# Performance work log

Hardware: AMD Instinct MI355X
Metric: run time of the kernel (lower is better)

The kernel has to match this reference:

```python
import jax, jax.numpy as jnp
import numpy as np

N, M, D = 8192, 8192, 256

def setup_inputs() -> dict:
    key = jax.random.key(0)
    kx, ky = jax.random.split(key)
    x = jax.random.normal(kx, (N, D), dtype=jnp.float32)
    y = jax.random.normal(ky, (M, D), dtype=jnp.float32)
    gamma = jnp.float32(1.0)  # learnable scalar parameter
    return {"x": x, "y": y, "gamma": gamma}

def reference(x, y, gamma):
    # Flatten trailing dims (matches x.view(x.size(0), -1))
    x = x.reshape(x.shape[0], -1)
    y = y.reshape(y.shape[0], -1)
    x_sq = jnp.sum(x * x, axis=-1)  # [N]
    y_sq = jnp.sum(y * y, axis=-1)  # [M]
    xy = x @ y.T                    # [N, M]
    sqdist = jnp.maximum(x_sq[:, None] + y_sq[None, :] - 2.0 * xy, 0.0)
    return jnp.exp(-gamma * sqdist)
```

## Files before the change

### kernel.cpp

```cpp
#include <hip/hip_runtime.h>
#include <stdint.h>


typedef __attribute__((ext_vector_type(4))) float f32x4;
typedef __attribute__((ext_vector_type(8))) int   i32x8;

#define NN 8192
#define MM 8192
#define DD 256
#define BK 128

__global__ __launch_bounds__(256) void prep_kernel(
    const float* __restrict__ x, const float* __restrict__ y,
    unsigned char* __restrict__ xb, unsigned char* __restrict__ yb,
    float* __restrict__ xsq, float* __restrict__ ysq) {
  const int lane = threadIdx.x & 63;
  const int row  = blockIdx.x * 4 + (threadIdx.x >> 6);

  const float* src = x;
  unsigned char* dst = xb;
  float* sq = xsq;
  int r = row;
  if (row >= NN) { src = y; dst = yb; sq = ysq; r = row - NN; }

  const float4 v = reinterpret_cast<const float4*>(src + (size_t)r * DD)[lane];
  float s = v.x * v.x + v.y * v.y + v.z * v.z + v.w * v.w;

  int w = 0;
  w = __builtin_amdgcn_cvt_pk_fp8_f32(v.x, v.y, w, false);
  w = __builtin_amdgcn_cvt_pk_fp8_f32(v.z, v.w, w, true);
  reinterpret_cast<int*>(dst + (size_t)r * DD)[lane] = w;

  #pragma unroll
  for (int o = 32; o > 0; o >>= 1) s += __shfl_down(s, o);
  if (lane == 0) sq[r] = s;
}

__global__ __launch_bounds__(256, 2) void rbf_gemm_kernel(
    const unsigned char* __restrict__ xb, const unsigned char* __restrict__ yb,
    const float* __restrict__ xsq, const float* __restrict__ ysq,
    const float* __restrict__ gamma, float* __restrict__ out) {
  __shared__ unsigned char As[128 * BK];
  __shared__ unsigned char Bs[128 * BK];

  const int tid   = threadIdx.x;
  const int lane  = tid & 63;
  const int wave  = tid >> 6;
  const int waveM = wave >> 1;
  const int waveN = wave & 1;
  const int row0  = blockIdx.y * 128;
  const int col0  = blockIdx.x * 128;

  f32x4 acc[4][4] = {};

  const int srow = lane >> 3;
  const int spos = lane & 7;
  const int sseg = ((spos & 1) | (((spos >> 1) ^ (srow & 3)) << 1)) * 16;

  const int fm = lane & 15;
  const int g  = lane >> 4;
  const int foff = fm * 128 + ((g ^ (fm & 3)) * 32);

  #pragma unroll
  for (int kt = 0; kt < 2; ++kt) {
    const int kk = kt * BK;
    __syncthreads();
    #pragma unroll
    for (int q = 0; q < 2; ++q) {
      const int c = wave * 2 + q;
      #pragma unroll
      for (int p = 0; p < 2; ++p) {
        const unsigned char* ga =
            yb + (size_t)(col0 + c * 16 + p * 8 + srow) * DD + kk + sseg;
        __builtin_amdgcn_global_load_lds(
            (const __attribute__((address_space(1))) void*)ga,
            (__attribute__((address_space(3))) void*)(As + c * 2048 + p * 1024),
            16, 0, 0);
        const unsigned char* gb =
            xb + (size_t)(row0 + c * 16 + p * 8 + srow) * DD + kk + sseg;
        __builtin_amdgcn_global_load_lds(
            (const __attribute__((address_space(1))) void*)gb,
            (__attribute__((address_space(3))) void*)(Bs + c * 2048 + p * 1024),
            16, 0, 0);
      }
    }
    __syncthreads();

    i32x8 a[4], b[4];
    #pragma unroll
    for (int i = 0; i < 4; ++i)
      a[i] = *reinterpret_cast<const i32x8*>(As + (waveM * 4 + i) * 2048 + foff);
    #pragma unroll
    for (int j = 0; j < 4; ++j)
      b[j] = *reinterpret_cast<const i32x8*>(Bs + (waveN * 4 + j) * 2048 + foff);

    #pragma unroll
    for (int i = 0; i < 4; ++i)
      #pragma unroll
      for (int j = 0; j < 4; ++j)
        acc[i][j] = __builtin_amdgcn_mfma_scale_f32_16x16x128_f8f6f4(
            a[i], b[j], acc[i][j], 0, 0,
            0, 0x7F7F7F7F, 0, 0x7F7F7F7F);
  }

  const float gm = gamma[0];
  const int rowb = row0 + waveN * 64 + (lane & 15);
  const int colq = col0 + waveM * 64 + (lane >> 4) * 4;

  float xsv[4];
  #pragma unroll
  for (int j = 0; j < 4; ++j) xsv[j] = xsq[rowb + j * 16];
  float4 ysv[4];
  #pragma unroll
  for (int i = 0; i < 4; ++i)
    ysv[i] = *reinterpret_cast<const float4*>(ysq + colq + i * 16);

  #pragma unroll
  for (int j = 0; j < 4; ++j) {
    const size_t obase = (size_t)(rowb + j * 16) * MM;
    #pragma unroll
    for (int i = 0; i < 4; ++i) {
      const float s0 = xsv[j] + ysv[i].x - 2.0f * acc[i][j][0];
      const float s1 = xsv[j] + ysv[i].y - 2.0f * acc[i][j][1];
      const float s2 = xsv[j] + ysv[i].z - 2.0f * acc[i][j][2];
      const float s3 = xsv[j] + ysv[i].w - 2.0f * acc[i][j][3];
      float4 v;
      const float mn = fminf(fminf(s0, s1), fminf(s2, s3));
      if (gm * mn >= 105.0f) {
        v.x = 0.0f; v.y = 0.0f; v.z = 0.0f; v.w = 0.0f;
      } else {
        v.x = __expf(-gm * fmaxf(s0, 0.0f));
        v.y = __expf(-gm * fmaxf(s1, 0.0f));
        v.z = __expf(-gm * fmaxf(s2, 0.0f));
        v.w = __expf(-gm * fmaxf(s3, 0.0f));
      }
      *reinterpret_cast<float4*>(out + obase + colq + i * 16) = v;
    }
  }
}

extern "C" void kernel_launch(void* const* d_in, const int* in_sizes, int n_in,
                              void* d_out, int out_size, void* d_ws, size_t ws_size,
                              hipStream_t stream) {
  const float* x     = (const float*)d_in[0];
  const float* y     = (const float*)d_in[1];
  const float* gamma = (const float*)d_in[2];
  float* out = (float*)d_out;

  unsigned char* xb = (unsigned char*)d_ws;
  unsigned char* yb = xb + (size_t)NN * DD;
  float* xsq = (float*)(yb + (size_t)MM * DD);
  float* ysq = xsq + NN;

  prep_kernel<<<(NN + MM) / 4, 256, 0, stream>>>(x, y, xb, yb, xsq, ysq);

  dim3 grid(MM / 128, NN / 128);
  rbf_gemm_kernel<<<grid, 256, 0, stream>>>(xb, yb, xsq, ysq, gamma, out);
}
```

Measured before the change: 287.1 us.

## Split output tile into two column halves and overlap second-half loads with first-half epilogue

Loads the full K=256 of the x tile and both K-halves of y into separate LDS buffers. The 128-column y tile is split into two 64-column halves, and the second half is issued as asynchronous global-to-LDS loads before the first half's compute and epilogue. The aim is to hide global load latency behind MFMA and exp/store work and to halve accumulator registers. It increases LDS use to 64KB per block, which may affect occupancy with the launch bound of 2 blocks, and B fragments are reloaded from LDS for each half.

```diff
diff --git a/kernel.cpp b/kernel.cpp
--- a/kernel.cpp
+++ b/kernel.cpp
@@ -8,7 +8,6 @@
 #define NN 8192
 #define MM 8192
 #define DD 256
-#define BK 128
 
 __global__ __launch_bounds__(256) void prep_kernel(
     const float* __restrict__ x, const float* __restrict__ y,
@@ -40,8 +39,8 @@
     const unsigned char* __restrict__ xb, const unsigned char* __restrict__ yb,
     const float* __restrict__ xsq, const float* __restrict__ ysq,
     const float* __restrict__ gamma, float* __restrict__ out) {
-  __shared__ unsigned char As[128 * BK];
-  __shared__ unsigned char Bs[128 * BK];
+  __shared__ unsigned char Bs[2][8 * 2048];
+  __shared__ unsigned char As[2][2][4 * 2048];
 
   const int tid   = threadIdx.x;
   const int lane  = tid & 63;
@@ -51,8 +50,6 @@
   const int row0  = blockIdx.y * 128;
   const int col0  = blockIdx.x * 128;
 
-  f32x4 acc[4][4] = {};
-
   const int srow = lane >> 3;
   const int spos = lane & 7;
   const int sseg = ((spos & 1) | (((spos >> 1) ^ (srow & 3)) << 1)) * 16;
@@ -61,82 +58,116 @@
   const int g  = lane >> 4;
   const int foff = fm * 128 + ((g ^ (fm & 3)) * 32);
 
-  #pragma unroll
-  for (int kt = 0; kt < 2; ++kt) {
-    const int kk = kt * BK;
-    __syncthreads();
+  auto stageB = [&](int kt) {
     #pragma unroll
     for (int q = 0; q < 2; ++q) {
       const int c = wave * 2 + q;
       #pragma unroll
       for (int p = 0; p < 2; ++p) {
-        const unsigned char* ga =
-            yb + (size_t)(col0 + c * 16 + p * 8 + srow) * DD + kk + sseg;
-        __builtin_amdgcn_global_load_lds(
-            (const __attribute__((address_space(1))) void*)ga,
-            (__attribute__((address_space(3))) void*)(As + c * 2048 + p * 1024),
-            16, 0, 0);
         const unsigned char* gb =
-            xb + (size_t)(row0 + c * 16 + p * 8 + srow) * DD + kk + sseg;
+            xb + (size_t)(row0 + c * 16 + p * 8 + srow) * DD + kt * 128 + sseg;
         __builtin_amdgcn_global_load_lds(
             (const __attribute__((address_space(1))) void*)gb,
-            (__attribute__((address_space(3))) void*)(Bs + c * 2048 + p * 1024),
+            (__attribute__((address_space(3))) void*)(Bs[kt] + c * 2048 + p * 1024),
             16, 0, 0);
       }
     }
-    __syncthreads();
+  };
+  auto stageA = [&](int h, int kt) {
+    const int c = wave;
+    #pragma unroll
+    for (int p = 0; p < 2; ++p) {
+      const unsigned char* ga =
+          yb + (size_t)(col0 + h * 64 + c * 16 + p * 8 + srow) * DD + kt * 128 + sseg;
+      __builtin_amdgcn_global_load_lds(
+          (const __attribute__((address_space(1))) void*)ga,
+          (__attribute__((address_space(3))) void*)(As[h][kt] + c * 2048 + p * 1024),
+          16, 0, 0);
+    }
+  };
 
-    i32x8 a[4], b[4];
-    #pragma unroll
-    for (int i = 0; i < 4; ++i)
-      a[i] = *reinterpret_cast<const i32x8*>(As + (waveM * 4 + i) * 2048 + foff);
-    #pragma unroll
-    for (int j = 0; j < 4; ++j)
-      b[j] = *reinterpret_cast<const i32x8*>(Bs + (waveN * 4 + j) * 2048 + foff);
-
-    #pragma unroll
-    for (int i = 0; i < 4; ++i)
-      #pragma unroll
-      for (int j = 0; j < 4; ++j)
-        acc[i][j] = __builtin_amdgcn_mfma_scale_f32_16x16x128_f8f6f4(
-            a[i], b[j], acc[i][j], 0, 0,
-            0, 0x7F7F7F7F, 0, 0x7F7F7F7F);
-  }
-
+  f32x4 acc[2][4];
   const float gm = gamma[0];
   const int rowb = row0 + waveN * 64 + (lane & 15);
-  const int colq = col0 + waveM * 64 + (lane >> 4) * 4;
 
   float xsv[4];
   #pragma unroll
   for (int j = 0; j < 4; ++j) xsv[j] = xsq[rowb + j * 16];
-  float4 ysv[4];
-  #pragma unroll
-  for (int i = 0; i < 4; ++i)
-    ysv[i] = *reinterpret_cast<const float4*>(ysq + colq + i * 16);
+
+  auto compute = [&](int h) {
+    #pragma unroll
+    for (int kt = 0; kt < 2; ++kt) {
+      i32x8 a[2], b[4];
+      #pragma unroll
+      for (int i = 0; i < 2; ++i)
+        a[i] = *reinterpret_cast<const i32x8*>(
+            As[h][kt] + (waveM * 2 + i) * 2048 + foff);
+      #pragma unroll
+      for (int j = 0; j < 4; ++j)
+        b[j] = *reinterpret_cast<const i32x8*>(
+            Bs[kt] + (waveN * 4 + j) * 2048 + foff);
+      #pragma unroll
+      for (int i = 0; i < 2; ++i)
+        #pragma unroll
+        for (int j = 0; j < 4; ++j)
+          acc[i][j] = __builtin_amdgcn_mfma_scale_f32_16x16x128_f8f6f4(
+              a[i], b[j], acc[i][j], 0, 0,
+              0, 0x7F7F7F7F, 0, 0x7F7F7F7F);
+    }
+  };
+  auto epilogue = [&](int h) {
+    const int colq = col0 + h * 64 + waveM * 32 + (lane >> 4) * 4;
+    float4 ysv[2];
+    #pragma unroll
+    for (int i = 0; i < 2; ++i)
+      ysv[i] = *reinterpret_cast<const float4*>(ysq + colq + i * 16);
+    #pragma unroll
+    for (int j = 0; j < 4; ++j) {
+      const size_t obase = (size_t)(rowb + j * 16) * MM;
+      #pragma unroll
+      for (int i = 0; i < 2; ++i) {
+        const float s0 = xsv[j] + ysv[i].x - 2.0f * acc[i][j][0];
+        const float s1 = xsv[j] + ysv[i].y - 2.0f * acc[i][j][1];
+        const float s2 = xsv[j] + ysv[i].z - 2.0f * acc[i][j][2];
+        const float s3 = xsv[j] + ysv[i].w - 2.0f * acc[i][j][3];
+        float4 v;
+        const float mn = fminf(fminf(s0, s1), fminf(s2, s3));
+        if (gm * mn >= 105.0f) {
+          v.x = 0.0f; v.y = 0.0f; v.z = 0.0f; v.w = 0.0f;
+        } else {
+          v.x = __expf(-gm * fmaxf(s0, 0.0f));
+          v.y = __expf(-gm * fmaxf(s1, 0.0f));
+          v.z = __expf(-gm * fmaxf(s2, 0.0f));
+          v.w = __expf(-gm * fmaxf(s3, 0.0f));
+        }
+        *reinterpret_cast<float4*>(out + obase + colq + i * 16) = v;
+      }
+    }
+  };
+
+  stageB(0); stageB(1);
+  stageA(0, 0); stageA(0, 1);
+  __syncthreads();
+
+  stageA(1, 0); stageA(1, 1);
 
   #pragma unroll
-  for (int j = 0; j < 4; ++j) {
-    const size_t obase = (size_t)(rowb + j * 16) * MM;
+  for (int i = 0; i < 2; ++i)
     #pragma unroll
-    for (int i = 0; i < 4; ++i) {
-      const float s0 = xsv[j] + ysv[i].x - 2.0f * acc[i][j][0];
-      const float s1 = xsv[j] + ysv[i].y - 2.0f * acc[i][j][1];
-      const float s2 = xsv[j] + ysv[i].z - 2.0f * acc[i][j][2];
-      const float s3 = xsv[j] + ysv[i].w - 2.0f * acc[i][j][3];
-      float4 v;
-      const float mn = fminf(fminf(s0, s1), fminf(s2, s3));
-      if (gm * mn >= 105.0f) {
-        v.x = 0.0f; v.y = 0.0f; v.z = 0.0f; v.w = 0.0f;
-      } else {
-        v.x = __expf(-gm * fmaxf(s0, 0.0f));
-        v.y = __expf(-gm * fmaxf(s1, 0.0f));
-        v.z = __expf(-gm * fmaxf(s2, 0.0f));
-        v.w = __expf(-gm * fmaxf(s3, 0.0f));
-      }
-      *reinterpret_cast<float4*>(out + obase + colq + i * 16) = v;
-    }
-  }
+    for (int j = 0; j < 4; ++j)
+      acc[i][j] = f32x4{0.f, 0.f, 0.f, 0.f};
+  compute(0);
+  epilogue(0);
+
+  __syncthreads();
+
+  #pragma unroll
+  for (int i = 0; i < 2; ++i)
+    #pragma unroll
+    for (int j = 0; j < 4; ++j)
+      acc[i][j] = f32x4{0.f, 0.f, 0.f, 0.f};
+  compute(1);
+  epilogue(1);
 }
 
 extern "C" void kernel_launch(void* const* d_in, const int* in_sizes, int n_in,
```

New measurement: 278.4 us (median of 2 runs). -3.1%, faster.

## Make GEMM blocks persistent over column strips with double-buffered y tiles

Applied to the files above, without the earlier changes.

Each block now keeps its x row tile in LDS and iterates over 8 column tiles, double-buffering y tile loads and overlapping the previous tile's exp epilogue and stores with the next loads and MFMAs. The grid shrinks to 512 blocks. This aims to hide global load latency and reuse the x tile, at the cost of larger LDS use and fewer blocks to spread across CUs.

```diff
diff --git a/kernel.cpp b/kernel.cpp
--- a/kernel.cpp
+++ b/kernel.cpp
@@ -8,7 +8,6 @@
 #define NN 8192
 #define MM 8192
 #define DD 256
-#define BK 128
 
 __global__ __launch_bounds__(256) void prep_kernel(
     const float* __restrict__ x, const float* __restrict__ y,
@@ -40,18 +39,18 @@
     const unsigned char* __restrict__ xb, const unsigned char* __restrict__ yb,
     const float* __restrict__ xsq, const float* __restrict__ ysq,
     const float* __restrict__ gamma, float* __restrict__ out) {
-  __shared__ unsigned char As[128 * BK];
-  __shared__ unsigned char Bs[128 * BK];
+  __shared__ unsigned char Bs[2][8 * 2048];
+  __shared__ unsigned char As[2][8 * 2048];
 
-  const int tid   = threadIdx.x;
-  const int lane  = tid & 63;
-  const int wave  = tid >> 6;
-  const int waveM = wave >> 1;
-  const int waveN = wave & 1;
-  const int row0  = blockIdx.y * 128;
-  const int col0  = blockIdx.x * 128;
-
-  f32x4 acc[4][4] = {};
+  const int tid    = threadIdx.x;
+  const int lane   = tid & 63;
+  const int wave   = tid >> 6;
+  const int waveM  = wave >> 1;
+  const int waveN  = wave & 1;
+  const int rowBlk = blockIdx.x & 63;
+  const int strip  = blockIdx.x >> 6;
+  const int row0   = rowBlk * 128;
+  const int cbase  = strip * 8 * 128;
 
   const int srow = lane >> 3;
   const int spos = lane & 7;
@@ -61,39 +60,55 @@
   const int g  = lane >> 4;
   const int foff = fm * 128 + ((g ^ (fm & 3)) * 32);
 
-  #pragma unroll
-  for (int kt = 0; kt < 2; ++kt) {
-    const int kk = kt * BK;
-    __syncthreads();
+  auto stageB = [&](int kt) {
+    #pragma unroll
+    for (int q = 0; q < 2; ++q) {
+      const int c = wave * 2 + q;
+      #pragma unroll
+      for (int p = 0; p < 2; ++p) {
+        const unsigned char* gb =
+            xb + (size_t)(row0 + c * 16 + p * 8 + srow) * DD + kt * 128 + sseg;
+        __builtin_amdgcn_global_load_lds(
+            (const __attribute__((address_space(1))) void*)gb,
+            (__attribute__((address_space(3))) void*)(Bs[kt] + c * 2048 + p * 1024),
+            16, 0, 0);
+      }
+    }
+  };
+  auto stageA = [&](int buf, int col0, int kt) {
     #pragma unroll
     for (int q = 0; q < 2; ++q) {
       const int c = wave * 2 + q;
       #pragma unroll
       for (int p = 0; p < 2; ++p) {
         const unsigned char* ga =
-            yb + (size_t)(col0 + c * 16 + p * 8 + srow) * DD + kk + sseg;
+            yb + (size_t)(col0 + c * 16 + p * 8 + srow) * DD + kt * 128 + sseg;
         __builtin_amdgcn_global_load_lds(
             (const __attribute__((address_space(1))) void*)ga,
-            (__attribute__((address_space(3))) void*)(As + c * 2048 + p * 1024),
-            16, 0, 0);
-        const unsigned char* gb =
-            xb + (size_t)(row0 + c * 16 + p * 8 + srow) * DD + kk + sseg;
-        __builtin_amdgcn_global_load_lds(
-            (const __attribute__((address_space(1))) void*)gb,
-            (__attribute__((address_space(3))) void*)(Bs + c * 2048 + p * 1024),
+            (__attribute__((address_space(3))) void*)(As[buf] + c * 2048 + p * 1024),
             16, 0, 0);
       }
     }
-    __syncthreads();
+  };
 
+  f32x4 acc[4][4];
+  const float gm   = gamma[0];
+  const int   rowb = row0 + waveN * 64 + (lane & 15);
+
+  float xsv[4];
+  #pragma unroll
+  for (int j = 0; j < 4; ++j) xsv[j] = xsq[rowb + j * 16];
+
+  auto compute = [&](int buf, int kt) {
     i32x8 a[4], b[4];
     #pragma unroll
     for (int i = 0; i < 4; ++i)
-      a[i] = *reinterpret_cast<const i32x8*>(As + (waveM * 4 + i) * 2048 + foff);
+      a[i] = *reinterpret_cast<const i32x8*>(
+          As[buf] + (waveM * 4 + i) * 2048 + foff);
     #pragma unroll
     for (int j = 0; j < 4; ++j)
-      b[j] = *reinterpret_cast<const i32x8*>(Bs + (waveN * 4 + j) * 2048 + foff);
-
+      b[j] = *reinterpret_cast<const i32x8*>(
+          Bs[kt] + (waveN * 4 + j) * 2048 + foff);
     #pragma unroll
     for (int i = 0; i < 4; ++i)
       #pragma unroll
@@ -101,42 +116,59 @@
         acc[i][j] = __builtin_amdgcn_mfma_scale_f32_16x16x128_f8f6f4(
             a[i], b[j], acc[i][j], 0, 0,
             0, 0x7F7F7F7F, 0, 0x7F7F7F7F);
+  };
+  auto epilogue = [&](int col0t) {
+    const int colq = col0t + waveM * 64 + (lane >> 4) * 4;
+    float4 ysv[4];
+    #pragma unroll
+    for (int i = 0; i < 4; ++i)
+      ysv[i] = *reinterpret_cast<const float4*>(ysq + colq + i * 16);
+    #pragma unroll
+    for (int j = 0; j < 4; ++j) {
+      const size_t obase = (size_t)(rowb + j * 16) * MM;
+      #pragma unroll
+      for (int i = 0; i < 4; ++i) {
+        const float s0 = xsv[j] + ysv[i].x - 2.0f * acc[i][j][0];
+        const float s1 = xsv[j] + ysv[i].y - 2.0f * acc[i][j][1];
+        const float s2 = xsv[j] + ysv[i].z - 2.0f * acc[i][j][2];
+        const float s3 = xsv[j] + ysv[i].w - 2.0f * acc[i][j][3];
+        float4 v;
+        const float mn = fminf(fminf(s0, s1), fminf(s2, s3));
+        if (gm * mn >= 105.0f) {
+          v.x = 0.0f; v.y = 0.0f; v.z = 0.0f; v.w = 0.0f;
+        } else {
+          v.x = __expf(-gm * fmaxf(s0, 0.0f));
+          v.y = __expf(-gm * fmaxf(s1, 0.0f));
+          v.z = __expf(-gm * fmaxf(s2, 0.0f));
+          v.w = __expf(-gm * fmaxf(s3, 0.0f));
+        }
+        *reinterpret_cast<float4*>(out + obase + colq + i * 16) = v;
+      }
+    }
+  };
+
+  stageB(0); stageB(1);
+  stageA(0, cbase, 0);
+  __syncthreads();
+
+  for (int t = 0; t < 8; ++t) {
+    const int c0 = cbase + t * 128;
+
+    stageA(1, c0, 1);
+    if (t) epilogue(c0 - 128);
+    #pragma unroll
+    for (int i = 0; i < 4; ++i)
+      #pragma unroll
+      for (int j = 0; j < 4; ++j)
+        acc[i][j] = f32x4{0.f, 0.f, 0.f, 0.f};
+    compute(0, 0);
+    __syncthreads();
+
+    if (t < 7) stageA(0, c0 + 128, 0);
+    compute(1, 1);
+    __syncthreads();
   }
-
-  const float gm = gamma[0];
-  const int rowb = row0 + waveN * 64 + (lane & 15);
-  const int colq = col0 + waveM * 64 + (lane >> 4) * 4;
-
-  float xsv[4];
-  #pragma unroll
-  for (int j = 0; j < 4; ++j) xsv[j] = xsq[rowb + j * 16];
-  float4 ysv[4];
-  #pragma unroll
-  for (int i = 0; i < 4; ++i)
-    ysv[i] = *reinterpret_cast<const float4*>(ysq + colq + i * 16);
-
-  #pragma unroll
-  for (int j = 0; j < 4; ++j) {
-    const size_t obase = (size_t)(rowb + j * 16) * MM;
-    #pragma unroll
-    for (int i = 0; i < 4; ++i) {
-      const float s0 = xsv[j] + ysv[i].x - 2.0f * acc[i][j][0];
-      const float s1 = xsv[j] + ysv[i].y - 2.0f * acc[i][j][1];
-      const float s2 = xsv[j] + ysv[i].z - 2.0f * acc[i][j][2];
-      const float s3 = xsv[j] + ysv[i].w - 2.0f * acc[i][j][3];
-      float4 v;
-      const float mn = fminf(fminf(s0, s1), fminf(s2, s3));
-      if (gm * mn >= 105.0f) {
-        v.x = 0.0f; v.y = 0.0f; v.z = 0.0f; v.w = 0.0f;
-      } else {
-        v.x = __expf(-gm * fmaxf(s0, 0.0f));
-        v.y = __expf(-gm * fmaxf(s1, 0.0f));
-        v.z = __expf(-gm * fmaxf(s2, 0.0f));
-        v.w = __expf(-gm * fmaxf(s3, 0.0f));
-      }
-      *reinterpret_cast<float4*>(out + obase + colq + i * 16) = v;
-    }
-  }
+  epilogue(cbase + 7 * 128);
 }
 
 extern "C" void kernel_launch(void* const* d_in, const int* in_sizes, int n_in,
@@ -154,6 +186,5 @@
 
   prep_kernel<<<(NN + MM) / 4, 256, 0, stream>>>(x, y, xb, yb, xsq, ysq);
 
-  dim3 grid(MM / 128, NN / 128);
-  rbf_gemm_kernel<<<grid, 256, 0, stream>>>(xb, yb, xsq, ysq, gamma, out);
+  rbf_gemm_kernel<<<512, 256, 0, stream>>>(xb, yb, xsq, ysq, gamma, out);
 }
```

Result: slower. 299.0 us (+4.1%).
